# Optimization experiments

Measured on AMD Instinct MI355X. Metric: run time of the kernel, lower is better.

The kernel has to match this reference:

```python
import jax, jax.numpy as jnp
import numpy as np

N_NODES = 50000
N_FRAMES = 5
N_EDGES = 400000
H1, C1 = 8, 8
D_MODEL = 64
N_HEADS, HEAD_DIM = 4, 16
EPS = 1e-5


def _gat_conv(h_in, src, dst, W, a_src, a_dst, heads, ch):
    # PyG GATConv (eval mode): linear -> per-head attn logits -> leaky_relu ->
    # segment softmax over incoming edges of each dst node -> weighted scatter-add.
    N = h_in.shape[0]
    h = (h_in @ W.T).reshape(N, heads, ch)            # [N,H,C]
    a_s = (h * a_src).sum(-1)                          # [N,H]
    a_d = (h * a_dst).sum(-1)                          # [N,H]
    e = jax.nn.leaky_relu(a_s[src] + a_d[dst], negative_slope=0.2)  # [E,H]
    e_max = jax.ops.segment_max(e, dst, num_segments=N)             # [N,H]
    ex = jnp.exp(e - e_max[dst])
    denom = jax.ops.segment_sum(ex, dst, num_segments=N)
    alpha = ex / denom[dst]                            # [E,H]
    return jax.ops.segment_sum(h[src] * alpha[..., None], dst, num_segments=N)  # [N,H,C]


def _ln(x, w, b):
    m = x.mean(-1, keepdims=True)
    v = ((x - m) ** 2).mean(-1, keepdims=True)
    return (x - m) / jnp.sqrt(v + EPS) * w + b


def _forward(x, edge_index, W1, att_src1, att_dst1, b1, W2, att_src2, att_dst2, b2,
             tWqkv, tbqkv, tWo, tbo, tln1w, tln1b, tWff1, tbff1, tWff2, tbff2,
             tln2w, tln2b, Wh1, bh1, Wh2, bh2):
    loops = jnp.arange(N_NODES, dtype=edge_index.dtype)  # add_self_loops=True
    embs = []
    for f in range(N_FRAMES):  # fixed small frame window
        src = jnp.concatenate([edge_index[f, 0], loops])
        dst = jnp.concatenate([edge_index[f, 1], loops])
        h = _gat_conv(x[f], src, dst, W1, att_src1, att_dst1, H1, C1).reshape(N_NODES, H1 * C1) + b1
        h = jax.nn.elu(h)
        h = _gat_conv(h, src, dst, W2, att_src2, att_dst2, 1, D_MODEL)[:, 0] + b2  # concat=False, 1 head
        embs.append(h.mean(0))  # graph embedding [64]
    seq = jnp.stack(embs)[None]  # [1,5,64]
    scale = 1.0 / np.sqrt(HEAD_DIM)
    for l in range(tWqkv.shape[0]):  # post-norm TransformerEncoderLayer (eval, relu)
        B, S, _ = seq.shape
        qkv = seq @ tWqkv[l].T + tbqkv[l]
        q, k, v = jnp.split(qkv, 3, axis=-1)
        q = q.reshape(B, S, N_HEADS, HEAD_DIM)
        k = k.reshape(B, S, N_HEADS, HEAD_DIM)
        v = v.reshape(B, S, N_HEADS, HEAD_DIM)
        att = jax.nn.softmax(jnp.einsum('bqhd,bkhd->bhqk', q, k) * scale, axis=-1)
        o = jnp.einsum('bhqk,bkhd->bqhd', att, v).reshape(B, S, D_MODEL)
        seq = _ln(seq + o @ tWo[l].T + tbo[l], tln1w[l], tln1b[l])
        ff = jax.nn.relu(seq @ tWff1[l].T + tbff1[l]) @ tWff2[l].T + tbff2[l]
        seq = _ln(seq + ff, tln2w[l], tln2b[l])
    last = seq[:, -1, :]
    return jax.nn.relu(last @ Wh1.T + bh1) @ Wh2.T + bh2  # [1,2]


def setup_inputs():
    key = jax.random.key(0)
    ks = jax.random.split(key, 16)
    p = lambda i, shape, s=0.1: jax.random.normal(ks[i], shape, dtype=jnp.float32) * s
    return {
        'x': jax.random.normal(ks[0], (N_FRAMES, N_NODES, 13), dtype=jnp.float32),
        'edge_index': jax.random.randint(ks[1], (N_FRAMES, 2, N_EDGES), 0, N_NODES, dtype=jnp.int32),
        'W1': p(2, (64, 13)), 'att_src1': p(3, (H1, C1)), 'att_dst1': p(4, (H1, C1)), 'b1': jnp.zeros((64,), jnp.float32),
        'W2': p(5, (64, 64)), 'att_src2': p(6, (1, 64)), 'att_dst2': p(7, (1, 64)), 'b2': jnp.zeros((64,), jnp.float32),
        'tWqkv': p(8, (3, 192, 64)), 'tbqkv': jnp.zeros((3, 192), jnp.float32),
        'tWo': p(9, (3, 64, 64)), 'tbo': jnp.zeros((3, 64), jnp.float32),
        'tln1w': jnp.ones((3, 64), jnp.float32), 'tln1b': jnp.zeros((3, 64), jnp.float32),
        'tWff1': p(10, (3, 128, 64)), 'tbff1': jnp.zeros((3, 128), jnp.float32),
        'tWff2': p(11, (3, 64, 128)), 'tbff2': jnp.zeros((3, 64), jnp.float32),
        'tln2w': jnp.ones((3, 64), jnp.float32), 'tln2b': jnp.zeros((3, 64), jnp.float32),
        'Wh1': p(12, (32, 64)), 'bh1': jnp.zeros((32,), jnp.float32),
        'Wh2': p(13, (2, 32)), 'bh2': jnp.zeros((2,), jnp.float32),
    }


def reference(x, edge_index, W1, att_src1, att_dst1, b1, W2, att_src2, att_dst2, b2,
              tWqkv, tbqkv, tWo, tbo, tln1w, tln1b, tWff1, tbff1, tWff2, tbff2,
              tln2w, tln2b, Wh1, bh1, Wh2, bh2):
    return _forward(x, edge_index, W1, att_src1, att_dst1, b1, W2, att_src2, att_dst2, b2,
                    tWqkv, tbqkv, tWo, tbo, tln1w, tln1b, tWff1, tbff1, tWff2, tbff2,
                    tln2w, tln2b, Wh1, bh1, Wh2, bh2)
```

## Files before the change

### kernel.cpp

```cpp
#include <hip/hip_runtime.h>
#include <math.h>

#define NN_F 50000
#define NE_F 400000
#define BPF  768

__device__ __forceinline__ float lrelu02(float x) { return x > 0.f ? x : 0.2f * x; }
__device__ __forceinline__ float fexp(float x) { return __expf(x); }

__device__ __forceinline__ unsigned short f2bf(float f) {
  unsigned int u = __float_as_uint(f);
  u += 0x7fffu + ((u >> 16) & 1u);
  return (unsigned short)(u >> 16);
}
__device__ __forceinline__ float bf_lo(unsigned int u) { return __uint_as_float(u << 16); }
__device__ __forceinline__ float bf_hi(unsigned int u) { return __uint_as_float(u & 0xffff0000u); }
__device__ __forceinline__ unsigned int pack2(float a, float b) {
  return (unsigned int)f2bf(a) | ((unsigned int)f2bf(b) << 16);
}

__global__ void __launch_bounds__(256, 3)
k_node1(const float* __restrict__ x, const float* __restrict__ W1,
        const float* __restrict__ attS, const float* __restrict__ attD,
        unsigned short* __restrict__ h1b, float* __restrict__ as1, float* __restrict__ ad1,
        int nNodes) {
  __shared__ float xbuf[4][16];
  int l = threadIdx.x & 63;
  int w = threadIdx.x >> 6;
  int wid = (blockIdx.x * blockDim.x + threadIdx.x) >> 6;
  int nw = (gridDim.x * blockDim.x) >> 6;
  float4 wA = make_float4(W1[l * 13 + 0], W1[l * 13 + 1], W1[l * 13 + 2], W1[l * 13 + 3]);
  float4 wB = make_float4(W1[l * 13 + 4], W1[l * 13 + 5], W1[l * 13 + 6], W1[l * 13 + 7]);
  float4 wC = make_float4(W1[l * 13 + 8], W1[l * 13 + 9], W1[l * 13 + 10], W1[l * 13 + 11]);
  float4 wD = make_float4(W1[l * 13 + 12], 0.f, 0.f, 0.f);
  float aS = attS[l], aD = attD[l];
  const float4* xb = reinterpret_cast<const float4*>(xbuf[w]);
  for (int n = wid; n < nNodes; n += nw) {
    if (l < 16) xbuf[w][l] = (l < 13) ? x[(size_t)n * 13 + l] : 0.f;
    float4 x0 = xb[0], x1 = xb[1], x2 = xb[2], x3 = xb[3];
    float a0 = x0.x * wA.x, a1 = x0.y * wA.y, a2 = x0.z * wA.z, a3 = x0.w * wA.w;
    a0 = fmaf(x1.x, wB.x, a0); a1 = fmaf(x1.y, wB.y, a1);
    a2 = fmaf(x1.z, wB.z, a2); a3 = fmaf(x1.w, wB.w, a3);
    a0 = fmaf(x2.x, wC.x, a0); a1 = fmaf(x2.y, wC.y, a1);
    a2 = fmaf(x2.z, wC.z, a2); a3 = fmaf(x2.w, wC.w, a3);
    a0 = fmaf(x3.x, wD.x, a0);
    float acc = (a0 + a1) + (a2 + a3);
    h1b[(size_t)n * 64 + l] = f2bf(acc);
    float s = acc * aS, d = acc * aD;
#pragma unroll
    for (int off = 1; off < 8; off <<= 1) {
      s += __shfl_xor(s, off, 64);
      d += __shfl_xor(d, off, 64);
    }
    if ((l & 7) == 0) { as1[n * 8 + (l >> 3)] = s; ad1[n * 8 + (l >> 3)] = d; }
  }
}

__global__ void k_rank(const int* __restrict__ ei, int* __restrict__ deg,
                       int* __restrict__ rank, int nFrames) {
  int tid = blockIdx.x * blockDim.x + threadIdx.x;
  int T = (nFrames * NE_F) >> 2;
  if (tid >= T) return;
  int gd[4];
#pragma unroll
  for (int i = 0; i < 4; i++) {
    int e = tid + i * T;
    int f = e / NE_F, idx = e - f * NE_F;
    gd[i] = f * NN_F + ei[(size_t)f * 2 * NE_F + NE_F + idx];
  }
  int r[4];
#pragma unroll
  for (int i = 0; i < 4; i++) r[i] = atomicAdd(&deg[gd[i]], 1);
#pragma unroll
  for (int i = 0; i < 4; i++) rank[tid + i * T] = r[i];
}

__global__ void k_scan1(const int* __restrict__ deg, int* __restrict__ bsum, int nNodes) {
  __shared__ int part[256];
  int t = threadIdx.x;
  int i = blockIdx.x * 256 + t;
  part[t] = (i < nNodes) ? deg[i] : 0;
  __syncthreads();
  for (int off = 128; off > 0; off >>= 1) {
    if (t < off) part[t] += part[t + off];
    __syncthreads();
  }
  if (t == 0) bsum[blockIdx.x] = part[0];
}

__global__ void __launch_bounds__(1024)
k_scan2(const int* __restrict__ bsum, int* __restrict__ boff, int nblk) {
  __shared__ int part[1024];
  int t = threadIdx.x;
  part[t] = (t < nblk) ? bsum[t] : 0;
  __syncthreads();
  for (int off = 1; off < 1024; off <<= 1) {
    int v = (t >= off) ? part[t - off] : 0;
    __syncthreads();
    part[t] += v;
    __syncthreads();
  }
  if (t < nblk) boff[t] = part[t] - bsum[t];
}

__global__ void k_scan3(const int* __restrict__ deg, const int* __restrict__ boff,
                        int* __restrict__ rowptr, int nNodes, int nEdges) {
  __shared__ int part[256];
  int t = threadIdx.x;
  int i = blockIdx.x * 256 + t;
  int d = (i < nNodes) ? deg[i] : 0;
  part[t] = d;
  __syncthreads();
  for (int off = 1; off < 256; off <<= 1) {
    int v = (t >= off) ? part[t - off] : 0;
    __syncthreads();
    part[t] += v;
    __syncthreads();
  }
  if (i < nNodes) rowptr[i] = boff[blockIdx.x] + part[t] - d;
  if (blockIdx.x == 0 && t == 0) rowptr[nNodes] = nEdges;
}

__global__ void k_place(const int* __restrict__ ei, const int* __restrict__ rowptr,
                        const int* __restrict__ rank, int* __restrict__ csr, int nFrames) {
  int tid = blockIdx.x * blockDim.x + threadIdx.x;
  int T = (nFrames * NE_F) >> 2;
  if (tid >= T) return;
#pragma unroll
  for (int i = 0; i < 4; i++) {
    int e = tid + i * T;
    int f = e / NE_F, idx = e - f * NE_F;
    const int* base = ei + (size_t)f * 2 * NE_F;
    int src = base[idx], dst = base[NE_F + idx];
    csr[rowptr[f * NN_F + dst] + rank[e]] = f * NN_F + src;
  }
}

__global__ void __launch_bounds__(256)
k_agg1(const int* __restrict__ rowptr, const int* __restrict__ csr,
       const unsigned short* __restrict__ h1b, const float* __restrict__ as1,
       const float* __restrict__ ad1, unsigned short* __restrict__ out1b, int nNodes) {
  int t = threadIdx.x;
  int l = t & 63;
  int grp = l >> 3, q = l & 7;
  int n = ((blockIdx.x * blockDim.x + t) >> 6) * 8 + grp;
  if (n >= nNodes) return;
  float adv = ad1[n * 8 + q];
  float e0 = fexp(lrelu02(as1[n * 8 + q] + adv));
  uint4 pv = *reinterpret_cast<const uint4*>(h1b + (size_t)n * 64 + q * 8);
  float a0 = e0 * bf_lo(pv.x), a1 = e0 * bf_hi(pv.x);
  float a2 = e0 * bf_lo(pv.y), a3 = e0 * bf_hi(pv.y);
  float a4 = e0 * bf_lo(pv.z), a5 = e0 * bf_hi(pv.z);
  float a6 = e0 * bf_lo(pv.w), a7 = e0 * bf_hi(pv.w);
  float den = e0;
  int s0 = rowptr[n], s1 = rowptr[n + 1];
  int i = s0;
  for (; i + 2 <= s1; i += 2) {
    int src0 = csr[i], src1 = csr[i + 1];
    float ea = fexp(lrelu02(as1[src0 * 8 + q] + adv));
    float eb = fexp(lrelu02(as1[src1 * 8 + q] + adv));
    uint4 va = *reinterpret_cast<const uint4*>(h1b + (size_t)src0 * 64 + q * 8);
    uint4 vb = *reinterpret_cast<const uint4*>(h1b + (size_t)src1 * 64 + q * 8);
    a0 = fmaf(ea, bf_lo(va.x), a0); a1 = fmaf(ea, bf_hi(va.x), a1);
    a2 = fmaf(ea, bf_lo(va.y), a2); a3 = fmaf(ea, bf_hi(va.y), a3);
    a4 = fmaf(ea, bf_lo(va.z), a4); a5 = fmaf(ea, bf_hi(va.z), a5);
    a6 = fmaf(ea, bf_lo(va.w), a6); a7 = fmaf(ea, bf_hi(va.w), a7);
    a0 = fmaf(eb, bf_lo(vb.x), a0); a1 = fmaf(eb, bf_hi(vb.x), a1);
    a2 = fmaf(eb, bf_lo(vb.y), a2); a3 = fmaf(eb, bf_hi(vb.y), a3);
    a4 = fmaf(eb, bf_lo(vb.z), a4); a5 = fmaf(eb, bf_hi(vb.z), a5);
    a6 = fmaf(eb, bf_lo(vb.w), a6); a7 = fmaf(eb, bf_hi(vb.w), a7);
    den += ea + eb;
  }
  if (i < s1) {
    int src = csr[i];
    float e2 = fexp(lrelu02(as1[src * 8 + q] + adv));
    uint4 v = *reinterpret_cast<const uint4*>(h1b + (size_t)src * 64 + q * 8);
    a0 = fmaf(e2, bf_lo(v.x), a0); a1 = fmaf(e2, bf_hi(v.x), a1);
    a2 = fmaf(e2, bf_lo(v.y), a2); a3 = fmaf(e2, bf_hi(v.y), a3);
    a4 = fmaf(e2, bf_lo(v.z), a4); a5 = fmaf(e2, bf_hi(v.z), a5);
    a6 = fmaf(e2, bf_lo(v.w), a6); a7 = fmaf(e2, bf_hi(v.w), a7);
    den += e2;
  }
  float inv = 1.f / den;
  uint4 o;
  o.x = pack2(a0 * inv, a1 * inv);
  o.y = pack2(a2 * inv, a3 * inv);
  o.z = pack2(a4 * inv, a5 * inv);
  o.w = pack2(a6 * inv, a7 * inv);
  *reinterpret_cast<uint4*>(out1b + (size_t)n * 64 + q * 8) = o;
}

__global__ void __launch_bounds__(256, 3)
k_node2(const unsigned short* __restrict__ out1b, const float* __restrict__ b1,
        const float* __restrict__ W2, const float* __restrict__ attS2,
        const float* __restrict__ attD2, unsigned short* __restrict__ gb,
        float* __restrict__ as2, float* __restrict__ ad2, int nNodes) {
  __shared__ float hbuf[4][64];
  int l = threadIdx.x & 63;
  int w = threadIdx.x >> 6;
  int wid = (blockIdx.x * blockDim.x + threadIdx.x) >> 6;
  int nw = (gridDim.x * blockDim.x) >> 6;
  const float4* W4 = reinterpret_cast<const float4*>(&W2[l * 64]);
  float4 w0 = W4[0],  w1 = W4[1],  w2 = W4[2],  w3 = W4[3];
  float4 w4 = W4[4],  w5 = W4[5],  w6 = W4[6],  w7 = W4[7];
  float4 w8 = W4[8],  w9 = W4[9],  w10 = W4[10], w11 = W4[11];
  float4 w12 = W4[12], w13 = W4[13], w14 = W4[14], w15 = W4[15];
  float aS = attS2[l], aD = attD2[l], bb = b1[l];
  const float4* hb = reinterpret_cast<const float4*>(hbuf[w]);
  for (int n = wid; n < nNodes; n += nw) {
    float v = __uint_as_float((unsigned int)out1b[(size_t)n * 64 + l] << 16) + bb;
    float hh = v > 0.f ? v : (fexp(v) - 1.f);
    hbuf[w][l] = hh;
    float a0 = 0.f, a1 = 0.f, a2 = 0.f, a3 = 0.f;
#define NSTEP(i, wv) { float4 hv = hb[i]; \
    a0 = fmaf(hv.x, wv.x, a0); a1 = fmaf(hv.y, wv.y, a1); \
    a2 = fmaf(hv.z, wv.z, a2); a3 = fmaf(hv.w, wv.w, a3); }
    NSTEP(0, w0)  NSTEP(1, w1)  NSTEP(2, w2)  NSTEP(3, w3)
    NSTEP(4, w4)  NSTEP(5, w5)  NSTEP(6, w6)  NSTEP(7, w7)
    NSTEP(8, w8)  NSTEP(9, w9)  NSTEP(10, w10) NSTEP(11, w11)
    NSTEP(12, w12) NSTEP(13, w13) NSTEP(14, w14) NSTEP(15, w15)
#undef NSTEP
    float acc = (a0 + a1) + (a2 + a3);
    gb[(size_t)n * 64 + l] = f2bf(acc);
    float s2 = acc * aS, d2 = acc * aD;
#pragma unroll
    for (int off = 32; off > 0; off >>= 1) {
      s2 += __shfl_xor(s2, off, 64);
      d2 += __shfl_xor(d2, off, 64);
    }
    if (l == 0) { as2[n] = s2; ad2[n] = d2; }
  }
}

__global__ void __launch_bounds__(256)
k_agg2mean(const int* __restrict__ rowptr, const int* __restrict__ csr,
           const unsigned short* __restrict__ gtab, const float* __restrict__ as2,
           const float* __restrict__ ad2, float* __restrict__ emb) {
  __shared__ float part[32][64];
  int t = threadIdx.x;
  int w = t >> 6, l = t & 63;
  int grp = l >> 3, q = l & 7;
  int f = blockIdx.x / BPF;
  int gf = (blockIdx.x - f * BPF) * 32 + w * 8 + grp;
  const int stride = BPF * 32;
  float m0 = 0.f, m1 = 0.f, m2 = 0.f, m3 = 0.f, m4 = 0.f, m5 = 0.f, m6 = 0.f, m7 = 0.f;
  for (int j = gf; j < NN_F; j += stride) {
    int n = f * NN_F + j;
    float adv = ad2[n];
    float e0 = fexp(lrelu02(as2[n] + adv));
    uint4 pv = *reinterpret_cast<const uint4*>(gtab + (size_t)n * 64 + q * 8);
    float a0 = e0 * bf_lo(pv.x), a1 = e0 * bf_hi(pv.x);
    float a2 = e0 * bf_lo(pv.y), a3 = e0 * bf_hi(pv.y);
    float a4 = e0 * bf_lo(pv.z), a5 = e0 * bf_hi(pv.z);
    float a6 = e0 * bf_lo(pv.w), a7 = e0 * bf_hi(pv.w);
    float den = e0;
    int s0 = rowptr[n], s1 = rowptr[n + 1];
    int i = s0;
    for (; i + 2 <= s1; i += 2) {
      int src0 = csr[i], src1 = csr[i + 1];
      float ea = fexp(lrelu02(as2[src0] + adv));
      float eb = fexp(lrelu02(as2[src1] + adv));
      uint4 va = *reinterpret_cast<const uint4*>(gtab + (size_t)src0 * 64 + q * 8);
      uint4 vb = *reinterpret_cast<const uint4*>(gtab + (size_t)src1 * 64 + q * 8);
      a0 = fmaf(ea, bf_lo(va.x), a0); a1 = fmaf(ea, bf_hi(va.x), a1);
      a2 = fmaf(ea, bf_lo(va.y), a2); a3 = fmaf(ea, bf_hi(va.y), a3);
      a4 = fmaf(ea, bf_lo(va.z), a4); a5 = fmaf(ea, bf_hi(va.z), a5);
      a6 = fmaf(ea, bf_lo(va.w), a6); a7 = fmaf(ea, bf_hi(va.w), a7);
      a0 = fmaf(eb, bf_lo(vb.x), a0); a1 = fmaf(eb, bf_hi(vb.x), a1);
      a2 = fmaf(eb, bf_lo(vb.y), a2); a3 = fmaf(eb, bf_hi(vb.y), a3);
      a4 = fmaf(eb, bf_lo(vb.z), a4); a5 = fmaf(eb, bf_hi(vb.z), a5);
      a6 = fmaf(eb, bf_lo(vb.w), a6); a7 = fmaf(eb, bf_hi(vb.w), a7);
      den += ea + eb;
    }
    if (i < s1) {
      int src = csr[i];
      float e2 = fexp(lrelu02(as2[src] + adv));
      uint4 v = *reinterpret_cast<const uint4*>(gtab + (size_t)src * 64 + q * 8);
      a0 = fmaf(e2, bf_lo(v.x), a0); a1 = fmaf(e2, bf_hi(v.x), a1);
      a2 = fmaf(e2, bf_lo(v.y), a2); a3 = fmaf(e2, bf_hi(v.y), a3);
      a4 = fmaf(e2, bf_lo(v.z), a4); a5 = fmaf(e2, bf_hi(v.z), a5);
      a6 = fmaf(e2, bf_lo(v.w), a6); a7 = fmaf(e2, bf_hi(v.w), a7);
      den += e2;
    }
    float inv = 1.f / den;
    m0 = fmaf(a0, inv, m0); m1 = fmaf(a1, inv, m1);
    m2 = fmaf(a2, inv, m2); m3 = fmaf(a3, inv, m3);
    m4 = fmaf(a4, inv, m4); m5 = fmaf(a5, inv, m5);
    m6 = fmaf(a6, inv, m6); m7 = fmaf(a7, inv, m7);
  }
  float4* pr = reinterpret_cast<float4*>(&part[w * 8 + grp][q * 8]);
  pr[0] = make_float4(m0, m1, m2, m3);
  pr[1] = make_float4(m4, m5, m6, m7);
  __syncthreads();
  if (t < 64) {
    float s = 0.f;
#pragma unroll
    for (int r = 0; r < 32; r++) s += part[r][t];
    atomicAdd(&emb[f * 64 + t], s * (1.0f / NN_F));
  }
}

__device__ __forceinline__ float grp16_reduce(float p) {
#pragma unroll
  for (int off = 1; off < 16; off <<= 1) p += __shfl_xor(p, off, 64);
  return p;
}

__global__ void __launch_bounds__(1024)
k_transformer(const float* __restrict__ emb, const float* __restrict__ b2,
              const float* __restrict__ Wqkv, const float* __restrict__ bqkv,
              const float* __restrict__ Wo, const float* __restrict__ bo,
              const float* __restrict__ ln1w, const float* __restrict__ ln1b,
              const float* __restrict__ Wff1, const float* __restrict__ bff1,
              const float* __restrict__ Wff2, const float* __restrict__ bff2,
              const float* __restrict__ ln2w, const float* __restrict__ ln2b,
              const float* __restrict__ Wh1, const float* __restrict__ bh1,
              const float* __restrict__ Wh2, const float* __restrict__ bh2,
              float* __restrict__ out) {
  __shared__ float seq[5][64];
  __shared__ float qkv[5][192];
  __shared__ float att[4][5][5];
  __shared__ float aob[5][64];
  __shared__ float ffb[5][128];
  __shared__ float tmp[5][64];
  __shared__ float hid[32];
  int t = threadIdx.x;
  int l = t & 63, w = t >> 6;
  int g = l >> 4, q = l & 15;

  if (t < 320) seq[t >> 6][t & 63] = emb[t] + b2[t & 63];
  __syncthreads();

  for (int ly = 0; ly < 3; ly++) {
    const float* Wq  = Wqkv + ly * 12288; const float* bq  = bqkv + ly * 192;
    const float* Wol = Wo   + ly * 4096;  const float* bol = bo   + ly * 64;
    const float* w1  = ln1w + ly * 64;    const float* bb1 = ln1b + ly * 64;
    const float* Wf1 = Wff1 + ly * 8192;  const float* bf1 = bff1 + ly * 128;
    const float* Wf2 = Wff2 + ly * 8192;  const float* bf2 = bff2 + ly * 64;
    const float* w2  = ln2w + ly * 64;    const float* bb2 = ln2b + ly * 64;

    for (int o = w * 4 + g; o < 960; o += 64) {
      int s = o / 192, j = o - s * 192;
      float4 wv = *reinterpret_cast<const float4*>(&Wq[j * 64 + q * 4]);
      float4 xv = *reinterpret_cast<const float4*>(&seq[s][q * 4]);
      float p = wv.x * xv.x + wv.y * xv.y + wv.z * xv.z + wv.w * xv.w;
      p = grp16_reduce(p);
      if (q == 0) qkv[s][j] = p + bq[j];
    }
    __syncthreads();

    if (t < 100) {
      int hh = t / 25, qs = (t / 5) % 5, ks = t % 5;
      float acc = 0.f;
      for (int d = 0; d < 16; d++)
        acc = fmaf(qkv[qs][hh * 16 + d], qkv[ks][64 + hh * 16 + d], acc);
      att[hh][qs][ks] = acc * 0.25f;
    }
    __syncthreads();
    if (t < 20) {
      int hh = t / 5, qs = t % 5;
      float m = att[hh][qs][0];
      for (int k2 = 1; k2 < 5; k2++) m = fmaxf(m, att[hh][qs][k2]);
      float ss = 0.f;
      for (int k2 = 0; k2 < 5; k2++) { float v = expf(att[hh][qs][k2] - m); att[hh][qs][k2] = v; ss += v; }
      float inv = 1.f / ss;
      for (int k2 = 0; k2 < 5; k2++) att[hh][qs][k2] *= inv;
    }
    __syncthreads();

    if (t < 320) {
      int s = t >> 6, j = t & 63, hh = j >> 4;
      float acc = 0.f;
      for (int k2 = 0; k2 < 5; k2++) acc = fmaf(att[hh][s][k2], qkv[k2][128 + j], acc);
      aob[s][j] = acc;
    }
    __syncthreads();

    for (int o = w * 4 + g; o < 320; o += 64) {
      int s = o >> 6, c = o & 63;
      float4 wv = *reinterpret_cast<const float4*>(&Wol[c * 64 + q * 4]);
      float4 xv = *reinterpret_cast<const float4*>(&aob[s][q * 4]);
      float p = wv.x * xv.x + wv.y * xv.y + wv.z * xv.z + wv.w * xv.w;
      p = grp16_reduce(p);
      if (q == 0) tmp[s][c] = seq[s][c] + p + bol[c];
    }
    __syncthreads();

    if (w < 5) {
      float v = tmp[w][l];
      float s1 = v, s2 = v * v;
#pragma unroll
      for (int off = 1; off < 64; off <<= 1) {
        s1 += __shfl_xor(s1, off, 64);
        s2 += __shfl_xor(s2, off, 64);
      }
      float m = s1 * (1.f / 64.f);
      float var = s2 * (1.f / 64.f) - m * m;
      float inv = 1.f / sqrtf(var + 1e-5f);
      seq[w][l] = (v - m) * inv * w1[l] + bb1[l];
    }
    __syncthreads();

    for (int o = w * 4 + g; o < 640; o += 64) {
      int s = o >> 7, j = o & 127;
      float4 wv = *reinterpret_cast<const float4*>(&Wf1[j * 64 + q * 4]);
      float4 xv = *reinterpret_cast<const float4*>(&seq[s][q * 4]);
      float p = wv.x * xv.x + wv.y * xv.y + wv.z * xv.z + wv.w * xv.w;
      p = grp16_reduce(p);
      if (q == 0) ffb[s][j] = fmaxf(p + bf1[j], 0.f);
    }
    __syncthreads();

    for (int o = w * 4 + g; o < 320; o += 64) {
      int s = o >> 6, c = o & 63;
      float4 wa = *reinterpret_cast<const float4*>(&Wf2[c * 128 + q * 8]);
      float4 wb = *reinterpret_cast<const float4*>(&Wf2[c * 128 + q * 8 + 4]);
      float4 xa = *reinterpret_cast<const float4*>(&ffb[s][q * 8]);
      float4 xb = *reinterpret_cast<const float4*>(&ffb[s][q * 8 + 4]);
      float p = wa.x * xa.x + wa.y * xa.y + wa.z * xa.z + wa.w * xa.w
              + wb.x * xb.x + wb.y * xb.y + wb.z * xb.z + wb.w * xb.w;
      p = grp16_reduce(p);
      if (q == 0) tmp[s][c] = seq[s][c] + p + bf2[c];
    }
    __syncthreads();

    if (w < 5) {
      float v = tmp[w][l];
      float s1 = v, s2 = v * v;
#pragma unroll
      for (int off = 1; off < 64; off <<= 1) {
        s1 += __shfl_xor(s1, off, 64);
        s2 += __shfl_xor(s2, off, 64);
      }
      float m = s1 * (1.f / 64.f);
      float var = s2 * (1.f / 64.f) - m * m;
      float inv = 1.f / sqrtf(var + 1e-5f);
      seq[w][l] = (v - m) * inv * w2[l] + bb2[l];
    }
    __syncthreads();
  }

  for (int o = w * 4 + g; o < 32; o += 64) {
    float4 wv = *reinterpret_cast<const float4*>(&Wh1[o * 64 + q * 4]);
    float4 xv = *reinterpret_cast<const float4*>(&seq[4][q * 4]);
    float p = wv.x * xv.x + wv.y * xv.y + wv.z * xv.z + wv.w * xv.w;
    p = grp16_reduce(p);
    if (q == 0) hid[o] = fmaxf(p + bh1[o], 0.f);
  }
  __syncthreads();
  if (t < 2) {
    float acc = bh2[t];
    for (int j = 0; j < 32; j++) acc = fmaf(hid[j], Wh2[t * 32 + j], acc);
    out[t] = acc;
  }
}

extern "C" void kernel_launch(void* const* d_in, const int* in_sizes, int n_in,
                              void* d_out, int out_size, void* d_ws, size_t ws_size,
                              hipStream_t stream) {
  const float* x     = (const float*)d_in[0];
  const int*   ei    = (const int*)d_in[1];
  const float* W1    = (const float*)d_in[2];
  const float* attS1 = (const float*)d_in[3];
  const float* attD1 = (const float*)d_in[4];
  const float* b1    = (const float*)d_in[5];
  const float* W2    = (const float*)d_in[6];
  const float* attS2 = (const float*)d_in[7];
  const float* attD2 = (const float*)d_in[8];
  const float* b2    = (const float*)d_in[9];
  const float* tWqkv = (const float*)d_in[10];
  const float* tbqkv = (const float*)d_in[11];
  const float* tWo   = (const float*)d_in[12];
  const float* tbo   = (const float*)d_in[13];
  const float* tln1w = (const float*)d_in[14];
  const float* tln1b = (const float*)d_in[15];
  const float* tWff1 = (const float*)d_in[16];
  const float* tbff1 = (const float*)d_in[17];
  const float* tWff2 = (const float*)d_in[18];
  const float* tbff2 = (const float*)d_in[19];
  const float* tln2w = (const float*)d_in[20];
  const float* tln2b = (const float*)d_in[21];
  const float* Wh1   = (const float*)d_in[22];
  const float* bh1   = (const float*)d_in[23];
  const float* Wh2   = (const float*)d_in[24];
  const float* bh2   = (const float*)d_in[25];
  float* out = (float*)d_out;

  auto need_bytes = [](int F) -> size_t {
    size_t NT = (size_t)F * NN_F, ET = (size_t)F * NE_F;
    size_t fl = NT * 18 + 320;
    size_t us = NT * 192;
    size_t it = NT * 2 + 1 + 2048 + ET * 2;
    return fl * 4 + us * 2 + it * 4;
  };
  const int F = (ws_size >= need_bytes(5)) ? 5 : 1;
  const int NT = F * NN_F, ET = F * NE_F;

  float* ws  = (float*)d_ws;
  float* as1 = ws;
  float* ad1 = as1 + (size_t)NT * 8;
  float* as2 = ad1 + (size_t)NT * 8;
  float* ad2 = as2 + NT;
  float* emb = ad2 + NT;
  unsigned short* h1b   = (unsigned short*)(emb + 320);
  unsigned short* gb    = h1b + (size_t)NT * 64;
  unsigned short* out1b = gb + (size_t)NT * 64;
  int* deg    = (int*)(out1b + (size_t)NT * 64);
  int* rowptr = deg + NT;
  int* bsum   = rowptr + NT + 1;
  int* boff   = bsum + 1024;
  int* rank   = boff + 1024;
  int* csr    = rank + ET;

  (void)hipMemsetAsync(emb, 0, 320 * sizeof(float), stream);

  const int nblk = (NT + 255) / 256;
  const int edge4Blocks = ((ET >> 2) + 255) / 256;
  const int agg1Blocks = (NT / 8 + 3) / 4;
  const int nodeBlocks = 2048;

  for (int f0 = 0; f0 < 5; f0 += F) {
    const float* xf = x + (size_t)f0 * NN_F * 13;
    const int* eif  = ei + (size_t)f0 * 2 * NE_F;

    (void)hipMemsetAsync(deg, 0, NT * sizeof(int), stream);
    k_rank<<<edge4Blocks, 256, 0, stream>>>(eif, deg, rank, F);
    k_scan1<<<nblk, 256, 0, stream>>>(deg, bsum, NT);
    k_scan2<<<1, 1024, 0, stream>>>(bsum, boff, nblk);
    k_scan3<<<nblk, 256, 0, stream>>>(deg, boff, rowptr, NT, ET);
    k_place<<<edge4Blocks, 256, 0, stream>>>(eif, rowptr, rank, csr, F);

    k_node1<<<nodeBlocks, 256, 0, stream>>>(xf, W1, attS1, attD1, h1b, as1, ad1, NT);
    k_agg1<<<agg1Blocks, 256, 0, stream>>>(rowptr, csr, h1b, as1, ad1, out1b, NT);
    k_node2<<<nodeBlocks, 256, 0, stream>>>(out1b, b1, W2, attS2, attD2, gb, as2, ad2, NT);
    k_agg2mean<<<F * BPF, 256, 0, stream>>>(rowptr, csr, gb, as2, ad2, emb + f0 * 64);
  }

  k_transformer<<<1, 1024, 0, stream>>>(emb, b2, tWqkv, tbqkv, tWo, tbo, tln1w, tln1b,
                                        tWff1, tbff1, tWff2, tbff2, tln2w, tln2b,
                                        Wh1, bh1, Wh2, bh2, out);
}
```

Baseline: 427.5 us.

## Compute second GAT linear layer with bf16 MFMA over 16-node tiles

Result: faster. 366.1 us (-14.4%).

```diff
diff --git a/kernel.cpp b/kernel.cpp
--- a/kernel.cpp
+++ b/kernel.cpp
@@ -18,6 +18,9 @@
 __device__ __forceinline__ unsigned int pack2(float a, float b) {
   return (unsigned int)f2bf(a) | ((unsigned int)f2bf(b) << 16);
 }
+
+typedef __attribute__((ext_vector_type(8))) short bfrag_t;
+typedef __attribute__((ext_vector_type(4))) float facc_t;
 
 __global__ void __launch_bounds__(256, 3)
 k_node1(const float* __restrict__ x, const float* __restrict__ W1,
@@ -190,45 +193,99 @@
   *reinterpret_cast<uint4*>(out1b + (size_t)n * 64 + q * 8) = o;
 }
 
-__global__ void __launch_bounds__(256, 3)
+__global__ void __launch_bounds__(256)
 k_node2(const unsigned short* __restrict__ out1b, const float* __restrict__ b1,
         const float* __restrict__ W2, const float* __restrict__ attS2,
         const float* __restrict__ attD2, unsigned short* __restrict__ gb,
         float* __restrict__ as2, float* __restrict__ ad2, int nNodes) {
-  __shared__ float hbuf[4][64];
-  int l = threadIdx.x & 63;
-  int w = threadIdx.x >> 6;
-  int wid = (blockIdx.x * blockDim.x + threadIdx.x) >> 6;
+  __shared__ unsigned short lg[4][16][72];
+  int t = threadIdx.x, l = t & 63, w = t >> 6;
+  int r16 = l & 15, g4 = l >> 4;
+
+  bfrag_t bfr[8];
+#pragma unroll
+  for (int tt = 0; tt < 4; tt++) {
+    const float* wrow = W2 + (tt * 16 + r16) * 64;
+#pragma unroll
+    for (int kc = 0; kc < 2; kc++) {
+      float4 lo = *reinterpret_cast<const float4*>(wrow + kc * 32 + 4 * g4);
+      float4 hi = *reinterpret_cast<const float4*>(wrow + kc * 32 + 16 + 4 * g4);
+      union { unsigned short u[8]; bfrag_t v; } pk;
+      pk.u[0] = f2bf(lo.x); pk.u[1] = f2bf(lo.y); pk.u[2] = f2bf(lo.z); pk.u[3] = f2bf(lo.w);
+      pk.u[4] = f2bf(hi.x); pk.u[5] = f2bf(hi.y); pk.u[6] = f2bf(hi.z); pk.u[7] = f2bf(hi.w);
+      bfr[tt * 2 + kc] = pk.v;
+    }
+  }
+  float4 bias[2][2];
+#pragma unroll
+  for (int kc = 0; kc < 2; kc++)
+#pragma unroll
+    for (int h = 0; h < 2; h++)
+      bias[kc][h] = *reinterpret_cast<const float4*>(b1 + kc * 32 + h * 16 + 4 * g4);
+  float aSr0 = attS2[r16], aSr1 = attS2[16 + r16], aSr2 = attS2[32 + r16], aSr3 = attS2[48 + r16];
+  float aDr0 = attD2[r16], aDr1 = attD2[16 + r16], aDr2 = attD2[32 + r16], aDr3 = attD2[48 + r16];
+
+  int wid = (blockIdx.x * blockDim.x + t) >> 6;
   int nw = (gridDim.x * blockDim.x) >> 6;
-  const float4* W4 = reinterpret_cast<const float4*>(&W2[l * 64]);
-  float4 w0 = W4[0],  w1 = W4[1],  w2 = W4[2],  w3 = W4[3];
-  float4 w4 = W4[4],  w5 = W4[5],  w6 = W4[6],  w7 = W4[7];
-  float4 w8 = W4[8],  w9 = W4[9],  w10 = W4[10], w11 = W4[11];
-  float4 w12 = W4[12], w13 = W4[13], w14 = W4[14], w15 = W4[15];
-  float aS = attS2[l], aD = attD2[l], bb = b1[l];
-  const float4* hb = reinterpret_cast<const float4*>(hbuf[w]);
-  for (int n = wid; n < nNodes; n += nw) {
-    float v = __uint_as_float((unsigned int)out1b[(size_t)n * 64 + l] << 16) + bb;
-    float hh = v > 0.f ? v : (fexp(v) - 1.f);
-    hbuf[w][l] = hh;
-    float a0 = 0.f, a1 = 0.f, a2 = 0.f, a3 = 0.f;
-#define NSTEP(i, wv) { float4 hv = hb[i]; \
-    a0 = fmaf(hv.x, wv.x, a0); a1 = fmaf(hv.y, wv.y, a1); \
-    a2 = fmaf(hv.z, wv.z, a2); a3 = fmaf(hv.w, wv.w, a3); }
-    NSTEP(0, w0)  NSTEP(1, w1)  NSTEP(2, w2)  NSTEP(3, w3)
-    NSTEP(4, w4)  NSTEP(5, w5)  NSTEP(6, w6)  NSTEP(7, w7)
-    NSTEP(8, w8)  NSTEP(9, w9)  NSTEP(10, w10) NSTEP(11, w11)
-    NSTEP(12, w12) NSTEP(13, w13) NSTEP(14, w14) NSTEP(15, w15)
-#undef NSTEP
-    float acc = (a0 + a1) + (a2 + a3);
-    gb[(size_t)n * 64 + l] = f2bf(acc);
-    float s2 = acc * aS, d2 = acc * aD;
-#pragma unroll
-    for (int off = 32; off > 0; off >>= 1) {
-      s2 += __shfl_xor(s2, off, 64);
-      d2 += __shfl_xor(d2, off, 64);
-    }
-    if (l == 0) { as2[n] = s2; ad2[n] = d2; }
+  int ntiles = nNodes >> 4;
+  for (int tile = wid; tile < ntiles; tile += nw) {
+    int n0 = tile << 4;
+    const unsigned short* arow = out1b + (size_t)(n0 + r16) * 64;
+    facc_t acc0 = 0, acc1 = 0, acc2 = 0, acc3 = 0;
+#pragma unroll
+    for (int kc = 0; kc < 2; kc++) {
+      union { unsigned short u[8]; bfrag_t v; } apk;
+#pragma unroll
+      for (int h = 0; h < 2; h++) {
+        uint2 raw = *reinterpret_cast<const uint2*>(arow + kc * 32 + h * 16 + 4 * g4);
+        float4 bb = bias[kc][h];
+        float f0 = bf_lo(raw.x) + bb.x, f1 = bf_hi(raw.x) + bb.y;
+        float f2 = bf_lo(raw.y) + bb.z, f3 = bf_hi(raw.y) + bb.w;
+        f0 = f0 > 0.f ? f0 : (fexp(f0) - 1.f);
+        f1 = f1 > 0.f ? f1 : (fexp(f1) - 1.f);
+        f2 = f2 > 0.f ? f2 : (fexp(f2) - 1.f);
+        f3 = f3 > 0.f ? f3 : (fexp(f3) - 1.f);
+        apk.u[h * 4 + 0] = f2bf(f0); apk.u[h * 4 + 1] = f2bf(f1);
+        apk.u[h * 4 + 2] = f2bf(f2); apk.u[h * 4 + 3] = f2bf(f3);
+      }
+      bfrag_t afr = apk.v;
+      acc0 = __builtin_amdgcn_mfma_f32_16x16x32_bf16(afr, bfr[0 * 2 + kc], acc0, 0, 0, 0);
+      acc1 = __builtin_amdgcn_mfma_f32_16x16x32_bf16(afr, bfr[1 * 2 + kc], acc1, 0, 0, 0);
+      acc2 = __builtin_amdgcn_mfma_f32_16x16x32_bf16(afr, bfr[2 * 2 + kc], acc2, 0, 0, 0);
+      acc3 = __builtin_amdgcn_mfma_f32_16x16x32_bf16(afr, bfr[3 * 2 + kc], acc3, 0, 0, 0);
+    }
+    float ps0 = acc0[0] * aSr0 + acc1[0] * aSr1 + acc2[0] * aSr2 + acc3[0] * aSr3;
+    float ps1 = acc0[1] * aSr0 + acc1[1] * aSr1 + acc2[1] * aSr2 + acc3[1] * aSr3;
+    float ps2 = acc0[2] * aSr0 + acc1[2] * aSr1 + acc2[2] * aSr2 + acc3[2] * aSr3;
+    float ps3 = acc0[3] * aSr0 + acc1[3] * aSr1 + acc2[3] * aSr2 + acc3[3] * aSr3;
+    float pd0 = acc0[0] * aDr0 + acc1[0] * aDr1 + acc2[0] * aDr2 + acc3[0] * aDr3;
+    float pd1 = acc0[1] * aDr0 + acc1[1] * aDr1 + acc2[1] * aDr2 + acc3[1] * aDr3;
+    float pd2 = acc0[2] * aDr0 + acc1[2] * aDr1 + acc2[2] * aDr2 + acc3[2] * aDr3;
+    float pd3 = acc0[3] * aDr0 + acc1[3] * aDr1 + acc2[3] * aDr2 + acc3[3] * aDr3;
+#pragma unroll
+    for (int off = 1; off < 16; off <<= 1) {
+      ps0 += __shfl_xor(ps0, off, 64); ps1 += __shfl_xor(ps1, off, 64);
+      ps2 += __shfl_xor(ps2, off, 64); ps3 += __shfl_xor(ps3, off, 64);
+      pd0 += __shfl_xor(pd0, off, 64); pd1 += __shfl_xor(pd1, off, 64);
+      pd2 += __shfl_xor(pd2, off, 64); pd3 += __shfl_xor(pd3, off, 64);
+    }
+    if (r16 == 0) {
+      *reinterpret_cast<float4*>(as2 + n0 + g4 * 4) = make_float4(ps0, ps1, ps2, ps3);
+      *reinterpret_cast<float4*>(ad2 + n0 + g4 * 4) = make_float4(pd0, pd1, pd2, pd3);
+    }
+#pragma unroll
+    for (int r = 0; r < 4; r++) {
+      lg[w][g4 * 4 + r][0 * 16 + r16] = f2bf(acc0[r]);
+      lg[w][g4 * 4 + r][1 * 16 + r16] = f2bf(acc1[r]);
+      lg[w][g4 * 4 + r][2 * 16 + r16] = f2bf(acc2[r]);
+      lg[w][g4 * 4 + r][3 * 16 + r16] = f2bf(acc3[r]);
+    }
+    asm volatile("s_waitcnt lgkmcnt(0)" ::: "memory");
+    int row = l >> 3, c = l & 7;
+    uint4 v0 = *reinterpret_cast<const uint4*>(&lg[w][row][c * 8]);
+    uint4 v1 = *reinterpret_cast<const uint4*>(&lg[w][8 + row][c * 8]);
+    *reinterpret_cast<uint4*>(gb + (size_t)(n0 + row) * 64 + c * 8) = v0;
+    *reinterpret_cast<uint4*>(gb + (size_t)(n0 + 8 + row) * 64 + c * 8) = v1;
   }
 }
 
@@ -518,6 +575,7 @@
   const int edge4Blocks = ((ET >> 2) + 255) / 256;
   const int agg1Blocks = (NT / 8 + 3) / 4;
   const int nodeBlocks = 2048;
+  const int node2Blocks = 1024;
 
   for (int f0 = 0; f0 < 5; f0 += F) {
     const float* xf = x + (size_t)f0 * NN_F * 13;
@@ -532,7 +590,7 @@
 
     k_node1<<<nodeBlocks, 256, 0, stream>>>(xf, W1, attS1, attD1, h1b, as1, ad1, NT);
     k_agg1<<<agg1Blocks, 256, 0, stream>>>(rowptr, csr, h1b, as1, ad1, out1b, NT);
-    k_node2<<<nodeBlocks, 256, 0, stream>>>(out1b, b1, W2, attS2, attD2, gb, as2, ad2, NT);
+    k_node2<<<node2Blocks, 256, 0, stream>>>(out1b, b1, W2, attS2, attD2, gb, as2, ad2, NT);
     k_agg2mean<<<F * BPF, 256, 0, stream>>>(rowptr, csr, gb, as2, ad2, emb + f0 * 64);
   }
 
```
